# Optimization experiments

Hardware: AMD Instinct MI355X
Metric: run time of the kernel (lower is better)

The kernel has to match this reference:

```python
import jax, jax.numpy as jnp
import numpy as np


def _pe_2d(H, W, C, dtype):
    # PositionalEncodingPermute2D: returns (C, H, W)
    ch_half = (C + 1) // 2
    inv = 1.0 / (10000.0 ** (jnp.arange(0, ch_half, 2, dtype=jnp.float32) / ch_half))
    tH = jnp.arange(H, dtype=jnp.float32)
    tW = jnp.arange(W, dtype=jnp.float32)
    sinH = tH[:, None] * inv[None, :]              # (H, ch_half//2)
    sinW = tW[:, None] * inv[None, :]              # (W, ch_half//2)
    embH = jnp.concatenate([jnp.sin(sinH), jnp.cos(sinH)], axis=-1)  # (H, ch_half)
    embW = jnp.concatenate([jnp.sin(sinW), jnp.cos(sinW)], axis=-1)  # (W, ch_half)
    E = jnp.concatenate([
        jnp.broadcast_to(embW[None, :, :], (H, W, ch_half)),
        jnp.broadcast_to(embH[:, None, :], (H, W, ch_half)),
    ], axis=-1)[..., :C]                            # (H, W, C)
    return jnp.transpose(E, (2, 0, 1)).astype(dtype)  # (C, H, W)


def setup_inputs() -> dict:
    key = jax.random.key(0)
    k0, k1, k2, k3 = jax.random.split(key, 4)
    B, C, H, W = 4, 256, 64, 64
    s = 1.0 / np.sqrt(C)  # kaiming-ish scale
    return {
        "x": jax.random.normal(k0, (B, C, H, W), dtype=jnp.float32),
        "wq": jax.random.normal(k1, (C, C), dtype=jnp.float32) * s,
        "wk": jax.random.normal(k2, (C, C), dtype=jnp.float32) * s,
        "wv": jax.random.normal(k3, (C, C), dtype=jnp.float32) * s,
    }


def reference(x, wq, wk, wv):
    B, C, H, W = x.shape
    scale = C ** (-0.5)
    x = x + _pe_2d(H, W, C, x.dtype)[None]          # (B, C, H, W)
    X = x.reshape(B, C, H * W).transpose(0, 2, 1)   # (B, N, C)
    Q = jnp.einsum('bnc,dc->bnd', X, wq)
    K = jnp.einsum('bnc,dc->bnd', X, wk)
    V = jnp.einsum('bnc,dc->bnd', X, wv)
    A = jax.nn.softmax(jnp.einsum('bnd,bmd->bnm', Q, K) * scale, axis=-1)
    Y = jnp.einsum('bnm,bmd->bnd', A, V)            # (B, N, C)
    return Y.transpose(0, 2, 1).reshape(B, C, H, W)
```

## Files before the change

### kernel.cpp

```cpp
#include <hip/hip_runtime.h>
#include <hip/hip_bf16.h>

#define BB 4
#define CC 256
#define NN 4096
#define NSPLIT 4
#define KSPLIT (NN / NSPLIT)
#define NT (KSPLIT / 32)

typedef __attribute__((ext_vector_type(8))) short short8;
typedef __attribute__((ext_vector_type(4))) float floatx4;
typedef __attribute__((ext_vector_type(4))) unsigned short ushortx4;

__device__ __forceinline__ float bf2f(unsigned short u) {
  union { unsigned int i; float f; } cv; cv.i = ((unsigned int)u) << 16; return cv.f;
}
__device__ __forceinline__ unsigned short f2bf(float f) {
  union { __hip_bfloat16 h; unsigned short u; } cv; cv.h = __float2bfloat16(f); return cv.u;
}

#define MFMA(a, b, c) __builtin_amdgcn_mfma_f32_16x16x32_bf16((a), (b), (c), 0, 0, 0)

__device__ __forceinline__ void dma16(const unsigned short* g, unsigned short* l) {
  __builtin_amdgcn_global_load_lds(
      (const __attribute__((address_space(1))) unsigned int*)g,
      (__attribute__((address_space(3))) unsigned int*)l, 16, 0, 0);
}
#define S_BARRIER __builtin_amdgcn_s_barrier()
#define MEMFENCE __asm__ volatile("" ::: "memory")

__global__ __launch_bounds__(256) void wcvt(const float* __restrict__ w0,
                                            const float* __restrict__ w1,
                                            const float* __restrict__ w2,
                                            unsigned short* __restrict__ o0,
                                            unsigned short* __restrict__ o1,
                                            unsigned short* __restrict__ o2) {
  const float* w = (blockIdx.y == 0) ? w0 : (blockIdx.y == 1) ? w1 : w2;
  unsigned short* o = (blockIdx.y == 0) ? o0 : (blockIdx.y == 1) ? o1 : o2;
  int i = (blockIdx.x * 256 + threadIdx.x) * 4;
  floatx4 v = *(const floatx4*)&w[i];
  ushortx4 p;
#pragma unroll
  for (int r = 0; r < 4; r++) p[r] = f2bf(v[r]);
  *(ushortx4*)&o[i] = p;
}

__global__ __launch_bounds__(256) void prep_x(const float* __restrict__ x,
                                              unsigned short* __restrict__ Xbf) {
  __shared__ float tile[32][33];
  int b = blockIdx.z;
  int n0 = blockIdx.x * 32, c0 = blockIdx.y * 32;
  int tx = threadIdx.x, ty = threadIdx.y;
#pragma unroll
  for (int i = 0; i < 4; i++) {
    int c = c0 + ty + i * 8;
    int n = n0 + tx;
    float v = x[((long)(b * CC + c)) * NN + n];
    int hh = n >> 6, ww = n & 63;
    int j = c & 63;
    float freq = exp2f(-0.2076205059304601f * (float)j);
    float arg = (float)((c < 128) ? ww : hh) * freq;
    v += (c & 64) ? cosf(arg) : sinf(arg);
    tile[ty + i * 8][tx] = v;
  }
  __syncthreads();
#pragma unroll
  for (int i = 0; i < 4; i++) {
    int n = n0 + ty + i * 8;
    int c = c0 + tx;
    Xbf[((long)(b * NN + n)) * CC + c] = f2bf(tile[tx][ty + i * 8]);
  }
}

__global__ __launch_bounds__(256, 2) void gemm_bt(const unsigned short* __restrict__ A, long asb,
                                                  const unsigned short* __restrict__ Bt, long bsb,
                                                  unsigned short* __restrict__ O, long osb,
                                                  int Nc) {
  __shared__ alignas(16) unsigned short Al[64][40];
  __shared__ alignas(16) unsigned short Bl[64][40];
  int b = blockIdx.z;
  const unsigned short* Ab = A + (long)b * asb;
  const unsigned short* Bb = Bt + (long)b * bsb;
  unsigned short* Ob = O + (long)b * osb;
  long row0 = (long)blockIdx.y * 64, col0 = (long)blockIdx.x * 64;
  int t = threadIdx.x, wave = t >> 6, lane = t & 63, quad = lane >> 4, l15 = lane & 15;
  int sr = t >> 2, sk = (t & 3) * 8;
  floatx4 acc[4] = {};
#pragma unroll
  for (int k0 = 0; k0 < 256; k0 += 32) {
    short8 av = *(const short8*)&Ab[(row0 + sr) * 256 + k0 + sk];
    short8 bv = *(const short8*)&Bb[(col0 + sr) * 256 + k0 + sk];
    __syncthreads();
    *(short8*)&Al[sr][sk] = av;
    *(short8*)&Bl[sr][sk] = bv;
    __syncthreads();
    short8 af = *(const short8*)&Al[wave * 16 + l15][quad * 8];
#pragma unroll
    for (int cb = 0; cb < 4; cb++) {
      short8 bf = *(const short8*)&Bl[cb * 16 + l15][quad * 8];
      acc[cb] = MFMA(af, bf, acc[cb]);
    }
  }
#pragma unroll
  for (int cb = 0; cb < 4; cb++) {
#pragma unroll
    for (int r = 0; r < 4; r++) {
      long row = row0 + wave * 16 + quad * 4 + r;
      long col = col0 + cb * 16 + l15;
      Ob[row * (long)Nc + col] = f2bf(acc[cb][r]);
    }
  }
}

__global__ __launch_bounds__(256, 2) void attn(const unsigned short* __restrict__ QKg,
                                               const unsigned short* __restrict__ Vtg,
                                               unsigned short* __restrict__ Opart,
                                               float* __restrict__ Lp) {
  __shared__ alignas(16) unsigned short Kl[2 * 8192];
  __shared__ alignas(16) unsigned short Vl[2 * 8192];
  __shared__ alignas(16) unsigned short Plf[4][2][512];
  int F = blockIdx.x;
  int c = F & 15, sp = c & 3, b = c >> 2;
  long q0 = (long)(F >> 4) * 128;
  int t = threadIdx.x, wave = t >> 6, lane = t & 63, quad = lane >> 4, l15 = lane & 15;
  const unsigned short* Qb = QKg + (long)b * NN * 512;
  const unsigned short* Kb = Qb + 256;
  const unsigned short* Vb = Vtg + (long)b * CC * NN;

  short8 qf[2][8];
#pragma unroll
  for (int qb = 0; qb < 2; qb++) {
    long qrow = q0 + wave * 32 + qb * 16 + l15;
#pragma unroll
    for (int ks = 0; ks < 8; ks++)
      qf[qb][ks] = *(const short8*)&Qb[qrow * 512 + ks * 32 + quad * 8];
  }

  floatx4 acc[2][17] = {};
  short8 ones;
#pragma unroll
  for (int j = 0; j < 8; j++) ones[j] = (short)0x3F80;

  const float sc = 0.0625f * 1.4426950408889634f;
  const int kbeg = sp * KSPLIT;

  auto stage = [&](int m0, int buf) {
#pragma unroll
    for (int st = 0; st < 4; st++) {
      int fg = st * 4 + wave;
      dma16(&Kb[(long)(m0 + (fg >> 3) * 16 + l15) * 512 + (fg & 7) * 32 + quad * 8],
            &Kl[buf * 8192 + fg * 512]);
      dma16(&Vb[(long)(fg * 16 + l15) * NN + m0 + quad * 8],
            &Vl[buf * 8192 + fg * 512]);
    }
  };

  __builtin_amdgcn_s_waitcnt(0xF70);
  stage(kbeg, 0);
  MEMFENCE;

  for (int i = 0; i < NT; i++) {
    int cur = i & 1;
    int m0 = kbeg + i * 32;
    S_BARRIER;
    MEMFENCE;
    if (i + 1 < NT) {
      stage(m0 + 32, cur ^ 1);
      MEMFENCE;
      __builtin_amdgcn_s_waitcnt(0xF78);
    } else {
      __builtin_amdgcn_s_waitcnt(0xF70);
    }
    S_BARRIER;
    MEMFENCE;

    int kb = cur * 8192;
    floatx4 s[2][2];
    {
      floatx4 z = {0.f, 0.f, 0.f, 0.f};
      s[0][0] = z; s[0][1] = z; s[1][0] = z; s[1][1] = z;
    }
#pragma unroll
    for (int fgk = 0; fgk < 16; fgk++) {
      short8 kf = *(const short8*)&Kl[kb + fgk * 512 + lane * 8];
      int mt = fgk >> 3, ks = fgk & 7;
      s[0][mt] = MFMA(qf[0][ks], kf, s[0][mt]);
      s[1][mt] = MFMA(qf[1][ks], kf, s[1][mt]);
    }

#pragma unroll
    for (int qb = 0; qb < 2; qb++) {
#pragma unroll
      for (int r = 0; r < 4; r++) {
        unsigned short pb0 = f2bf(exp2f(s[qb][0][r] * sc));
        unsigned short pb1 = f2bf(exp2f(s[qb][1][r] * sc));
        int m = quad * 4 + r;
        Plf[wave][qb][((l15 >> 3) * 16 + m) * 8 + (l15 & 7)] = pb0;
        Plf[wave][qb][((2 + (l15 >> 3)) * 16 + m) * 8 + (l15 & 7)] = pb1;
      }
    }
    MEMFENCE;
    short8 pf0 = *(const short8*)&Plf[wave][0][lane * 8];
    short8 pf1 = *(const short8*)&Plf[wave][1][lane * 8];
    acc[0][16] = MFMA(pf0, ones, acc[0][16]);
    acc[1][16] = MFMA(pf1, ones, acc[1][16]);
#pragma unroll
    for (int db = 0; db < 16; db++) {
      short8 vf = *(const short8*)&Vl[kb + db * 512 + lane * 8];
      acc[0][db] = MFMA(pf0, vf, acc[0][db]);
      acc[1][db] = MFMA(pf1, vf, acc[1][db]);
    }
  }

  unsigned short* Ob = Opart + (long)(b * NSPLIT + sp) * CC * NN;
#pragma unroll
  for (int qb = 0; qb < 2; qb++) {
    long nidx = q0 + wave * 32 + qb * 16 + quad * 4;
#pragma unroll
    for (int db = 0; db < 16; db++) {
      long d = db * 16 + l15;
      ushortx4 pk;
#pragma unroll
      for (int r = 0; r < 4; r++) pk[r] = f2bf(acc[qb][db][r]);
      *(ushortx4*)&Ob[d * NN + nidx] = pk;
    }
    if (l15 == 0) {
#pragma unroll
      for (int r = 0; r < 4; r++)
        Lp[(long)(b * NSPLIT + sp) * NN + nidx + r] = acc[qb][16][r];
    }
  }
}

__global__ __launch_bounds__(256) void combine(const unsigned short* __restrict__ Op,
                                               const float* __restrict__ Lp,
                                               float* __restrict__ Out) {
  __shared__ float Wl[64];
  int b = blockIdx.z;
  int d0 = blockIdx.y * 64, n0 = blockIdx.x * 64;
  int t = threadIdx.x;
  if (t < 64) {
    int n = n0 + t;
    float L = 0.f;
#pragma unroll
    for (int s = 0; s < NSPLIT; s++) L += Lp[(long)(b * NSPLIT + s) * NN + n];
    Wl[t] = 1.0f / L;
  }
  __syncthreads();
  int tn = t & 15, td = t >> 4;
  int nb = n0 + tn * 4;
  float w[4];
#pragma unroll
  for (int r = 0; r < 4; r++) w[r] = Wl[tn * 4 + r];
#pragma unroll
  for (int dd = 0; dd < 4; dd++) {
    int d = d0 + td * 4 + dd;
    floatx4 o = {0.f, 0.f, 0.f, 0.f};
#pragma unroll
    for (int s = 0; s < NSPLIT; s++) {
      ushortx4 pv = *(const ushortx4*)&Op[((long)(b * NSPLIT + s) * CC + d) * NN + nb];
#pragma unroll
      for (int r = 0; r < 4; r++) o[r] += bf2f(pv[r]);
    }
#pragma unroll
    for (int r = 0; r < 4; r++) o[r] *= w[r];
    *(floatx4*)&Out[((long)b * CC + d) * NN + nb] = o;
  }
}

extern "C" void kernel_launch(void* const* d_in, const int* in_sizes, int n_in,
                              void* d_out, int out_size, void* d_ws, size_t ws_size,
                              hipStream_t stream) {
  const float* x = (const float*)d_in[0];
  const float* wq = (const float*)d_in[1];
  const float* wk = (const float*)d_in[2];
  const float* wv = (const float*)d_in[3];
  float* out = (float*)d_out;

  char* ws = (char*)d_ws;
  unsigned short* QKbuf = (unsigned short*)(ws);
  unsigned short* Vt = (unsigned short*)(ws + (16l << 20));
  unsigned short* Xbf = (unsigned short*)(ws + (24l << 20));
  unsigned short* Opart = (unsigned short*)(ws + (24l << 20));
  float* Lp = (float*)(ws + (56l << 20));
  unsigned short* Wqk = (unsigned short*)(ws + (57l << 20));
  unsigned short* Wv = (unsigned short*)(ws + (57l << 20) + (1 << 19));

  wcvt<<<dim3(CC * CC / 1024, 3), 256, 0, stream>>>(wq, wk, wv, Wqk, Wqk + CC * CC, Wv);
  prep_x<<<dim3(NN / 32, CC / 32, BB), dim3(32, 8), 0, stream>>>(x, Xbf);
  gemm_bt<<<dim3(512 / 64, NN / 64, BB), 256, 0, stream>>>(Xbf, (long)NN * CC, Wqk, 0, QKbuf,
                                                           (long)NN * 512, 512);
  gemm_bt<<<dim3(NN / 64, CC / 64, BB), 256, 0, stream>>>(Wv, 0, Xbf, (long)NN * CC, Vt,
                                                          (long)CC * NN, NN);
  attn<<<dim3(512), 256, 0, stream>>>(QKbuf, Vt, Opart, Lp);
  combine<<<dim3(NN / 64, CC / 64, BB), 256, 0, stream>>>(Opart, Lp, out);
}
```

Before: 217.7 us.

## Enlarge attention blocks to 8 waves and stage two key tiles per barrier

```diff
diff --git a/kernel.cpp b/kernel.cpp
--- a/kernel.cpp
+++ b/kernel.cpp
@@ -6,7 +6,7 @@
 #define NN 4096
 #define NSPLIT 4
 #define KSPLIT (NN / NSPLIT)
-#define NT (KSPLIT / 32)
+#define NPAIR (KSPLIT / 64)
 
 typedef __attribute__((ext_vector_type(8))) short short8;
 typedef __attribute__((ext_vector_type(4))) float floatx4;
@@ -112,16 +112,16 @@
   }
 }
 
-__global__ __launch_bounds__(256, 2) void attn(const unsigned short* __restrict__ QKg,
+__global__ __launch_bounds__(512, 1) void attn(const unsigned short* __restrict__ QKg,
                                                const unsigned short* __restrict__ Vtg,
                                                unsigned short* __restrict__ Opart,
                                                float* __restrict__ Lp) {
-  __shared__ alignas(16) unsigned short Kl[2 * 8192];
-  __shared__ alignas(16) unsigned short Vl[2 * 8192];
-  __shared__ alignas(16) unsigned short Plf[4][2][512];
+  __shared__ alignas(16) unsigned short Kl[4 * 8192];
+  __shared__ alignas(16) unsigned short Vl[4 * 8192];
+  __shared__ alignas(16) unsigned short Plf[8][2][512];
   int F = blockIdx.x;
   int c = F & 15, sp = c & 3, b = c >> 2;
-  long q0 = (long)(F >> 4) * 128;
+  long q0 = (long)(F >> 4) * 256;
   int t = threadIdx.x, wave = t >> 6, lane = t & 63, quad = lane >> 4, l15 = lane & 15;
   const unsigned short* Qb = QKg + (long)b * NN * 512;
   const unsigned short* Kb = Qb + 256;
@@ -144,28 +144,32 @@
   const float sc = 0.0625f * 1.4426950408889634f;
   const int kbeg = sp * KSPLIT;
 
-  auto stage = [&](int m0, int buf) {
-#pragma unroll
-    for (int st = 0; st < 4; st++) {
-      int fg = st * 4 + wave;
-      dma16(&Kb[(long)(m0 + (fg >> 3) * 16 + l15) * 512 + (fg & 7) * 32 + quad * 8],
-            &Kl[buf * 8192 + fg * 512]);
-      dma16(&Vb[(long)(fg * 16 + l15) * NN + m0 + quad * 8],
-            &Vl[buf * 8192 + fg * 512]);
+  auto stage_pair = [&](int p, int buf) {
+#pragma unroll
+    for (int tt = 0; tt < 2; tt++) {
+      int m0 = kbeg + (p * 2 + tt) * 64 / 2;
+      int slot = buf * 2 + tt;
+#pragma unroll
+      for (int st = 0; st < 2; st++) {
+        int fg = st * 8 + wave;
+        dma16(&Kb[(long)(m0 + st * 16 + l15) * 512 + wave * 32 + quad * 8],
+              &Kl[slot * 8192 + fg * 512]);
+        dma16(&Vb[(long)(fg * 16 + l15) * NN + m0 + quad * 8],
+              &Vl[slot * 8192 + fg * 512]);
+      }
     }
   };
 
   __builtin_amdgcn_s_waitcnt(0xF70);
-  stage(kbeg, 0);
+  stage_pair(0, 0);
   MEMFENCE;
 
-  for (int i = 0; i < NT; i++) {
-    int cur = i & 1;
-    int m0 = kbeg + i * 32;
+  for (int p = 0; p < NPAIR; p++) {
+    int buf = p & 1;
     S_BARRIER;
     MEMFENCE;
-    if (i + 1 < NT) {
-      stage(m0 + 32, cur ^ 1);
+    if (p + 1 < NPAIR) {
+      stage_pair(p + 1, buf ^ 1);
       MEMFENCE;
       __builtin_amdgcn_s_waitcnt(0xF78);
     } else {
@@ -174,41 +178,45 @@
     S_BARRIER;
     MEMFENCE;
 
-    int kb = cur * 8192;
-    floatx4 s[2][2];
-    {
-      floatx4 z = {0.f, 0.f, 0.f, 0.f};
-      s[0][0] = z; s[0][1] = z; s[1][0] = z; s[1][1] = z;
-    }
-#pragma unroll
-    for (int fgk = 0; fgk < 16; fgk++) {
-      short8 kf = *(const short8*)&Kl[kb + fgk * 512 + lane * 8];
-      int mt = fgk >> 3, ks = fgk & 7;
-      s[0][mt] = MFMA(qf[0][ks], kf, s[0][mt]);
-      s[1][mt] = MFMA(qf[1][ks], kf, s[1][mt]);
-    }
-
-#pragma unroll
-    for (int qb = 0; qb < 2; qb++) {
-#pragma unroll
-      for (int r = 0; r < 4; r++) {
-        unsigned short pb0 = f2bf(exp2f(s[qb][0][r] * sc));
-        unsigned short pb1 = f2bf(exp2f(s[qb][1][r] * sc));
-        int m = quad * 4 + r;
-        Plf[wave][qb][((l15 >> 3) * 16 + m) * 8 + (l15 & 7)] = pb0;
-        Plf[wave][qb][((2 + (l15 >> 3)) * 16 + m) * 8 + (l15 & 7)] = pb1;
-      }
-    }
-    MEMFENCE;
-    short8 pf0 = *(const short8*)&Plf[wave][0][lane * 8];
-    short8 pf1 = *(const short8*)&Plf[wave][1][lane * 8];
-    acc[0][16] = MFMA(pf0, ones, acc[0][16]);
-    acc[1][16] = MFMA(pf1, ones, acc[1][16]);
-#pragma unroll
-    for (int db = 0; db < 16; db++) {
-      short8 vf = *(const short8*)&Vl[kb + db * 512 + lane * 8];
-      acc[0][db] = MFMA(pf0, vf, acc[0][db]);
-      acc[1][db] = MFMA(pf1, vf, acc[1][db]);
+#pragma unroll
+    for (int tt = 0; tt < 2; tt++) {
+      int kb = (buf * 2 + tt) * 8192;
+      floatx4 s[2][2];
+      {
+        floatx4 z = {0.f, 0.f, 0.f, 0.f};
+        s[0][0] = z; s[0][1] = z; s[1][0] = z; s[1][1] = z;
+      }
+#pragma unroll
+      for (int fgk = 0; fgk < 16; fgk++) {
+        short8 kf = *(const short8*)&Kl[kb + fgk * 512 + lane * 8];
+        int mt = fgk >> 3, ks = fgk & 7;
+        s[0][mt] = MFMA(qf[0][ks], kf, s[0][mt]);
+        s[1][mt] = MFMA(qf[1][ks], kf, s[1][mt]);
+      }
+
+#pragma unroll
+      for (int qb = 0; qb < 2; qb++) {
+#pragma unroll
+        for (int r = 0; r < 4; r++) {
+          unsigned short pb0 = f2bf(__builtin_amdgcn_exp2f(s[qb][0][r] * sc));
+          unsigned short pb1 = f2bf(__builtin_amdgcn_exp2f(s[qb][1][r] * sc));
+          int m = quad * 4 + r;
+          Plf[wave][qb][((l15 >> 3) * 16 + m) * 8 + (l15 & 7)] = pb0;
+          Plf[wave][qb][((2 + (l15 >> 3)) * 16 + m) * 8 + (l15 & 7)] = pb1;
+        }
+      }
+      MEMFENCE;
+      short8 pf0 = *(const short8*)&Plf[wave][0][lane * 8];
+      short8 pf1 = *(const short8*)&Plf[wave][1][lane * 8];
+      acc[0][16] = MFMA(pf0, ones, acc[0][16]);
+      acc[1][16] = MFMA(pf1, ones, acc[1][16]);
+#pragma unroll
+      for (int db = 0; db < 16; db++) {
+        short8 vf = *(const short8*)&Vl[kb + db * 512 + lane * 8];
+        acc[0][db] = MFMA(pf0, vf, acc[0][db]);
+        acc[1][db] = MFMA(pf1, vf, acc[1][db]);
+      }
+      MEMFENCE;
     }
   }
 
@@ -292,6 +300,6 @@
                                                            (long)NN * 512, 512);
   gemm_bt<<<dim3(NN / 64, CC / 64, BB), 256, 0, stream>>>(Wv, 0, Xbf, (long)NN * CC, Vt,
                                                           (long)CC * NN, NN);
-  attn<<<dim3(512), 256, 0, stream>>>(QKbuf, Vt, Opart, Lp);
+  attn<<<dim3(256), 512, 0, stream>>>(QKbuf, Vt, Opart, Lp);
   combine<<<dim3(NN / 64, CC / 64, BB), 256, 0, stream>>>(Opart, Lp, out);
 }
```

Result: faster. 201.0 us (-7.6%).
